# Kernel optimization log

Measured on AMD Instinct MI355X. Metric: run time of the kernel, lower is better.

Reference implementation:

```python
import jax, jax.numpy as jnp
import numpy as np

N = 20000
IN_CH, HID, OUT_CH = 512, 64, 16
H1, H2 = 8, 1
NEG_SLOPE = 0.2


def setup_inputs() -> dict:
    key = jax.random.key(0)
    ks = jax.random.split(key, 10)
    E = 320000
    x = jax.random.normal(ks[0], (N, IN_CH), dtype=jnp.float32)
    edge_index = jax.random.randint(ks[1], (2, E), 0, N, dtype=jnp.int64)
    s = 0.05
    return {
        "x": x,
        "edge_index": edge_index,
        "W1": jax.random.normal(ks[2], (H1 * HID, IN_CH), dtype=jnp.float32) * s,
        "att_src1": jax.random.normal(ks[3], (1, H1, HID), dtype=jnp.float32) * s,
        "att_dst1": jax.random.normal(ks[4], (1, H1, HID), dtype=jnp.float32) * s,
        "b1": jnp.zeros((H1 * HID,), dtype=jnp.float32),
        "W2": jax.random.normal(ks[5], (H2 * OUT_CH, H1 * HID), dtype=jnp.float32) * s,
        "att_src2": jax.random.normal(ks[6], (1, H2, OUT_CH), dtype=jnp.float32) * s,
        "att_dst2": jax.random.normal(ks[7], (1, H2, OUT_CH), dtype=jnp.float32) * s,
        "b2": jnp.zeros((OUT_CH,), dtype=jnp.float32),
    }


def _gat_conv(x, src, dst, W, att_src, att_dst, bias, heads, out_ch, concat):
    # Linear transform: [N, H, C]
    h = (x @ W.T).reshape(x.shape[0], heads, out_ch)
    n = x.shape[0]
    # Per-node attention logits (a_src . h), (a_dst . h): [N, H]
    a_s = (h * att_src).sum(-1)
    a_d = (h * att_dst).sum(-1)
    # Edge-wise LeakyReLU attention: [E, H]
    e = a_s[src] + a_d[dst]
    e = jnp.where(e >= 0, e, NEG_SLOPE * e)
    # Segment softmax over incoming edges of each destination node
    m = jax.ops.segment_max(e, dst, num_segments=n)
    p = jnp.exp(e - m[dst])
    z = jax.ops.segment_sum(p, dst, num_segments=n)
    alpha = p / z[dst]  # [E, H]
    # Weighted scatter-aggregate: out[dst] += alpha * h[src]
    msg = h[src] * alpha[:, :, None]  # [E, H, C]
    out = jax.ops.segment_sum(msg, dst, num_segments=n)
    out = out.reshape(n, heads * out_ch) if concat else out.mean(axis=1)
    return out + bias


def reference(x, edge_index, W1, att_src1, att_dst1, b1, W2, att_src2, att_dst2, b2):
    # PyG GATConv adds self-loops by default
    loops = jnp.arange(N, dtype=edge_index.dtype)
    src = jnp.concatenate([edge_index[0], loops])
    dst = jnp.concatenate([edge_index[1], loops])
    # dropout layers are identity in eval mode
    h = _gat_conv(x, src, dst, W1, att_src1, att_dst1, b1, H1, HID, True)
    h = jax.nn.relu(h)
    out = _gat_conv(h, src, dst, W2, att_src2, att_dst2, b2, H2, OUT_CH, False)
    return out
```

## Files before the change

### kernel.cpp

```cpp
#include <hip/hip_runtime.h>

#define Nn     20000
#define IN_CH  512
#define C1     512
#define H1n    8
#define HIDn   64
#define OUT_CH 16
#define En     320000
#define EPn    340000
#define NEG    0.2f

typedef __attribute__((ext_vector_type(8))) short bf16x8;
typedef __attribute__((ext_vector_type(4))) float f32x4;

__device__ inline unsigned short bf16_rne(float f) {
  unsigned int u = __float_as_uint(f);
  return (unsigned short)((u + 0x7fffu + ((u >> 16) & 1u)) >> 16);
}
__device__ inline float bf16_f(unsigned short u) {
  return __uint_as_float(((unsigned int)u) << 16);
}

#define NX8  (Nn * IN_CH / 8)
#define NW8  (C1 * IN_CH / 8)
#define NW28 (OUT_CH * C1 / 8)
__global__ __launch_bounds__(256) void cvt3_kernel(
    const float* __restrict__ x,  unsigned short* __restrict__ xb,
    const float* __restrict__ W1, unsigned short* __restrict__ w1b,
    const float* __restrict__ W2, unsigned short* __restrict__ w2b)
{
  int i = blockIdx.x * 256 + threadIdx.x;
  const float* in; unsigned short* ob; int idx;
  if (i < NX8) { in = x; ob = xb; idx = i; }
  else if (i < NX8 + NW8) { in = W1; ob = w1b; idx = i - NX8; }
  else if (i < NX8 + NW8 + NW28) { in = W2; ob = w2b; idx = i - NX8 - NW8; }
  else return;
  float4 f0 = ((const float4*)in)[idx * 2];
  float4 f1 = ((const float4*)in)[idx * 2 + 1];
  float f[8] = {f0.x, f0.y, f0.z, f0.w, f1.x, f1.y, f1.z, f1.w};
  unsigned short h[8];
#pragma unroll
  for (int j = 0; j < 8; j++) h[j] = bf16_rne(f[j]);
  ushort4 hv0 = {h[0], h[1], h[2], h[3]}, hv1 = {h[4], h[5], h[6], h[7]};
  ((ushort4*)ob)[idx * 2] = hv0; ((ushort4*)ob)[idx * 2 + 1] = hv1;
}

#define GLL(gp, lp) __builtin_amdgcn_global_load_lds( \
    (const __attribute__((address_space(1))) void*)(gp), \
    (__attribute__((address_space(3))) void*)(lp), 16, 0, 0)

#define SWZ(c) ((c) ^ (((c) >> 3) & 3))

__global__ __launch_bounds__(256, 2) void gemm1_mfma(
    const unsigned short* __restrict__ Ab, const unsigned short* __restrict__ Bb,
    const float* __restrict__ attS, const float* __restrict__ attD,
    unsigned short* __restrict__ Cb, float* __restrict__ as1, float* __restrict__ ad1)
{
  __shared__ unsigned short sA[128 * 32], sB[128 * 32];
  int t = threadIdx.x;
  int bm = blockIdx.x, bn = blockIdx.y;
  int lane = t & 63, w = t >> 6;

  int slot0 = w * 128 + lane;
  int slot1 = slot0 + 64;
  int cb0 = w * 128, cb1 = w * 128 + 64;
  int cs0 = SWZ(slot0), cs1 = SWZ(slot1);
  int ar0 = bm * 128 + (cs0 >> 2); if (ar0 > Nn - 1) ar0 = Nn - 1;
  int ar1 = bm * 128 + (cs1 >> 2); if (ar1 > Nn - 1) ar1 = Nn - 1;
  int br0 = bn * 128 + (cs0 >> 2);
  int br1 = bn * 128 + (cs1 >> 2);
  size_t offA0 = (size_t)ar0 * IN_CH + (cs0 & 3) * 8;
  size_t offA1 = (size_t)ar1 * IN_CH + (cs1 & 3) * 8;
  size_t offB0 = (size_t)br0 * IN_CH + (cs0 & 3) * 8;
  size_t offB1 = (size_t)br1 * IN_CH + (cs1 & 3) * 8;

  int wm = (w >> 1) * 64, wn = (w & 1) * 64;
  int lr = lane & 15, kb = lane >> 4;

  f32x4 acc[4][4] = {};

  for (int k0 = 0; k0 < IN_CH; k0 += 32) {
    __syncthreads();
    GLL(Ab + offA0 + k0, sA + cb0 * 8);
    GLL(Ab + offA1 + k0, sA + cb1 * 8);
    GLL(Bb + offB0 + k0, sB + cb0 * 8);
    GLL(Bb + offB1 + k0, sB + cb1 * 8);
    __syncthreads();

    bf16x8 ah[4], bh[4];
#pragma unroll
    for (int i = 0; i < 4; i++) {
      int rca = (wm + i * 16 + lr) * 4 + kb;
      ah[i] = *(const bf16x8*)&sA[SWZ(rca) * 8];
      int rcb = (wn + i * 16 + lr) * 4 + kb;
      bh[i] = *(const bf16x8*)&sB[SWZ(rcb) * 8];
    }
#pragma unroll
    for (int i = 0; i < 4; i++)
#pragma unroll
      for (int j = 0; j < 4; j++)
        acc[i][j] = __builtin_amdgcn_mfma_f32_16x16x32_bf16(ah[i], bh[j], acc[i][j], 0, 0, 0);
  }

  int lq = lane >> 4;
#pragma unroll
  for (int i = 0; i < 4; i++) {
    int r0 = bm * 128 + wm + i * 16 + lq * 4;
#pragma unroll
    for (int j = 0; j < 4; j++) {
      int cc = bn * 128 + wn + j * 16 + lr;
#pragma unroll
      for (int q = 0; q < 4; q++) {
        int r = r0 + q;
        if (r < Nn) Cb[(size_t)r * C1 + cc] = bf16_rne(acc[i][j][q]);
      }
    }
  }
  int hh = bn * 2 + (wn >> 6);
  float aSj[4], aDj[4];
#pragma unroll
  for (int j = 0; j < 4; j++) {
    int cc = bn * 128 + wn + j * 16 + lr;
    aSj[j] = attS[cc]; aDj[j] = attD[cc];
  }
#pragma unroll
  for (int i = 0; i < 4; i++)
#pragma unroll
    for (int q = 0; q < 4; q++) {
      float s = acc[i][0][q] * aSj[0] + acc[i][1][q] * aSj[1]
              + acc[i][2][q] * aSj[2] + acc[i][3][q] * aSj[3];
      float dd = acc[i][0][q] * aDj[0] + acc[i][1][q] * aDj[1]
               + acc[i][2][q] * aDj[2] + acc[i][3][q] * aDj[3];
#pragma unroll
      for (int off = 1; off < 16; off <<= 1) {
        s += __shfl_xor(s, off);
        dd += __shfl_xor(dd, off);
      }
      int r = bm * 128 + wm + i * 16 + lq * 4 + q;
      if (lr == 0 && r < Nn) { as1[r * 8 + hh] = s; ad1[r * 8 + hh] = dd; }
    }
}

__global__ void hist_kernel(const int* __restrict__ ei, int* __restrict__ cnt)
{
  int e = blockIdx.x * 256 + threadIdx.x;
  if (e >= EPn) return;
  int d = (e < En) ? ei[En + e] : (e - En);
  atomicAdd(&cnt[d], 1);
}

__global__ __launch_bounds__(1024) void scan_kernel(
    const int* __restrict__ cnt, int* __restrict__ row)
{
  __shared__ int wsum[16];
  int t = threadIdx.x;
  int base = t * 20;
  int v[20];
  int s = 0;
#pragma unroll
  for (int j = 0; j < 20; j++) {
    int i = base + j;
    int c = (i < Nn) ? cnt[i] : 0;
    v[j] = s;
    s += c;
  }
  int lane = t & 63, w = t >> 6;
  int incl = s;
#pragma unroll
  for (int off = 1; off < 64; off <<= 1) {
    int o = __shfl_up(incl, off);
    if (lane >= off) incl += o;
  }
  if (lane == 63) wsum[w] = incl;
  __syncthreads();
  if (w == 0) {
    int ws = (lane < 16) ? wsum[lane] : 0;
#pragma unroll
    for (int off = 1; off < 16; off <<= 1) {
      int o = __shfl_up(ws, off);
      if (lane >= off) ws += o;
    }
    if (lane < 16) wsum[lane] = ws;
  }
  __syncthreads();
  int excl = ((w > 0) ? wsum[w - 1] : 0) + incl - s;
#pragma unroll
  for (int j = 0; j < 20; j++) {
    int i = base + j;
    if (i < Nn) row[i] = excl + v[j];
  }
  if (t == 0) row[Nn] = EPn;
}

__global__ void scatter_kernel(const int* __restrict__ ei, const int* __restrict__ row,
                               int* __restrict__ cur, int* __restrict__ csr)
{
  int e = blockIdx.x * 256 + threadIdx.x;
  if (e >= EPn) return;
  int s, d;
  if (e < En) { s = ei[e]; d = ei[En + e]; }
  else        { s = e - En; d = e - En; }
  int pos = row[d] + atomicAdd(&cur[d], 1);
  csr[pos] = s;
}

__global__ __launch_bounds__(256) void agg1_kernel(
    const int* __restrict__ row, const int* __restrict__ csr,
    const unsigned short* __restrict__ h1b, const float* __restrict__ as1,
    const float* __restrict__ adv, const float* __restrict__ b1,
    unsigned short* __restrict__ outb)
{
  int wv = threadIdx.x >> 6, lane = threadIdx.x & 63;
  int d = blockIdx.x * 4 + wv;
  int beg = row[d], end = row[d + 1];
  int hq = lane >> 3;
  size_t chb = (size_t)8 * lane;
  float adH = adv[d * 8 + hq];

  float a0 = 0.f, a1 = 0.f, a2 = 0.f, a3 = 0.f;
  float a4 = 0.f, a5 = 0.f, a6 = 0.f, a7 = 0.f;
  float z = 0.f;
#pragma unroll 4
  for (int e = beg; e < end; e++) {
    int s = csr[e];
    float v = as1[s * 8 + hq] + adH;
    v = (v >= 0.f) ? v : NEG * v;
    float p = __expf(v);
    z += p;
    uint4 u = *(const uint4*)&h1b[(size_t)s * C1 + chb];
    a0 = fmaf(p, __uint_as_float(u.x << 16), a0);
    a1 = fmaf(p, __uint_as_float(u.x & 0xffff0000u), a1);
    a2 = fmaf(p, __uint_as_float(u.y << 16), a2);
    a3 = fmaf(p, __uint_as_float(u.y & 0xffff0000u), a3);
    a4 = fmaf(p, __uint_as_float(u.z << 16), a4);
    a5 = fmaf(p, __uint_as_float(u.z & 0xffff0000u), a5);
    a6 = fmaf(p, __uint_as_float(u.w << 16), a6);
    a7 = fmaf(p, __uint_as_float(u.w & 0xffff0000u), a7);
  }

  float rz = 1.f / z;
  float4 b0 = *(const float4*)&b1[chb];
  float4 b4 = *(const float4*)&b1[chb + 4];
  float o[8] = {fmaf(a0, rz, b0.x), fmaf(a1, rz, b0.y),
                fmaf(a2, rz, b0.z), fmaf(a3, rz, b0.w),
                fmaf(a4, rz, b4.x), fmaf(a5, rz, b4.y),
                fmaf(a6, rz, b4.z), fmaf(a7, rz, b4.w)};
  unsigned short r[8];
#pragma unroll
  for (int i = 0; i < 8; i++) r[i] = bf16_rne(o[i] > 0.f ? o[i] : 0.f);
  ushort4 r0 = {r[0], r[1], r[2], r[3]}, r4 = {r[4], r[5], r[6], r[7]};
  *(ushort4*)&outb[(size_t)d * C1 + chb] = r0;
  *(ushort4*)&outb[(size_t)d * C1 + chb + 4] = r4;
}

__global__ __launch_bounds__(256) void l2_mfma(
    const unsigned short* __restrict__ Xb, const unsigned short* __restrict__ W2b,
    const float* __restrict__ att_s, const float* __restrict__ att_d,
    float* __restrict__ h2, float* __restrict__ as2, float* __restrict__ ad2)
{
  int w = threadIdx.x >> 6, lane = threadIdx.x & 63;
  int tile = blockIdx.x * 4 + w;
  if (tile >= Nn / 16) return;
  int n0 = tile * 16;
  int lr = lane & 15, kb = lane >> 4;

  bf16x8 bf[16];
#pragma unroll
  for (int k0 = 0; k0 < 16; k0++)
    bf[k0] = *(const bf16x8*)&W2b[lr * 512 + kb * 8 + k0 * 32];

  f32x4 acc = {0.f, 0.f, 0.f, 0.f};
#pragma unroll
  for (int k0 = 0; k0 < 16; k0++) {
    bf16x8 af = *(const bf16x8*)&Xb[(size_t)(n0 + lr) * 512 + kb * 8 + k0 * 32];
    acc = __builtin_amdgcn_mfma_f32_16x16x32_bf16(af, bf[k0], acc, 0, 0, 0);
  }

  float aS = att_s[lr], aD = att_d[lr];
#pragma unroll
  for (int r = 0; r < 4; r++) {
    int n = n0 + kb * 4 + r;
    h2[(size_t)n * 16 + lr] = acc[r];
    float sv = acc[r] * aS, dv = acc[r] * aD;
#pragma unroll
    for (int off = 1; off < 16; off <<= 1) {
      sv += __shfl_xor(sv, off);
      dv += __shfl_xor(dv, off);
    }
    if (lr == 0) { as2[n] = sv; ad2[n] = dv; }
  }
}

__global__ __launch_bounds__(256) void agg2_kernel(
    const int* __restrict__ row, const int* __restrict__ csr,
    const float* __restrict__ h2, const float* __restrict__ as2,
    const float* __restrict__ ad2, const float* __restrict__ b2,
    float* __restrict__ out)
{
  int wave = threadIdx.x >> 6, lane = threadIdx.x & 63;
  int d = blockIdx.x * 4 + wave;
  int beg = row[d], end = row[d + 1];
  float add = ad2[d];

  int c = lane & 15;
  float acc = 0.f, z = 0.f;
  for (int e = beg + (lane >> 4); e < end; e += 4) {
    int s = csr[e];
    float v = as2[s] + add;
    v = (v >= 0.f) ? v : NEG * v;
    float p = __expf(v);
    z += p;
    acc = fmaf(p, h2[(size_t)s * 16 + c], acc);
  }
  acc += __shfl_xor(acc, 16);
  acc += __shfl_xor(acc, 32);
  z += __shfl_xor(z, 16);
  z += __shfl_xor(z, 32);
  if (lane < 16) out[(size_t)d * 16 + lane] = acc / z + b2[lane];
}

extern "C" void kernel_launch(void* const* d_in, const int* in_sizes, int n_in,
                              void* d_out, int out_size, void* d_ws, size_t ws_size,
                              hipStream_t stream)
{
  const float* x    = (const float*)d_in[0];
  const int*   ei   = (const int*)d_in[1];
  const float* W1   = (const float*)d_in[2];
  const float* asv1 = (const float*)d_in[3];
  const float* adv1 = (const float*)d_in[4];
  const float* b1   = (const float*)d_in[5];
  const float* W2   = (const float*)d_in[6];
  const float* asv2 = (const float*)d_in[7];
  const float* adv2 = (const float*)d_in[8];
  const float* b2   = (const float*)d_in[9];
  float* out = (float*)d_out;

  unsigned short* h1b    = (unsigned short*)d_ws;
  unsigned short* relu1b = h1b + (size_t)Nn * C1;
  unsigned short* w_b    = relu1b + (size_t)Nn * C1;
  unsigned short* w2b    = w_b + (size_t)C1 * IN_CH;
  float* as1   = (float*)(w2b + (size_t)OUT_CH * C1);
  float* ad1   = as1 + (size_t)Nn * H1n;
  float* h2    = ad1 + (size_t)Nn * H1n;
  float* as2   = h2 + (size_t)Nn * OUT_CH;
  float* ad2   = as2 + Nn;
  int* csr  = (int*)(ad2 + Nn);
  int* cnt  = csr + EPn;
  int* rowp = cnt + Nn;
  int* cur  = rowp + Nn + 1;

  unsigned short* x_b = (unsigned short*)relu1b;

  hipMemsetAsync(cnt, 0, Nn * sizeof(int), stream);
  hipMemsetAsync(cur, 0, Nn * sizeof(int), stream);

  cvt3_kernel<<<(NX8 + NW8 + NW28 + 255) / 256, 256, 0, stream>>>(
      x, x_b, W1, w_b, W2, w2b);

  dim3 g1(157, 4);
  gemm1_mfma<<<g1, 256, 0, stream>>>(x_b, w_b, asv1, adv1, h1b, as1, ad1);

  hist_kernel<<<(EPn + 255) / 256, 256, 0, stream>>>(ei, cnt);
  scan_kernel<<<1, 1024, 0, stream>>>(cnt, rowp);
  scatter_kernel<<<(EPn + 255) / 256, 256, 0, stream>>>(ei, rowp, cur, csr);
  agg1_kernel<<<Nn / 4, 256, 0, stream>>>(rowp, csr, h1b, as1, ad1, b1, relu1b);
  l2_mfma<<<(Nn / 16 + 3) / 4, 256, 0, stream>>>(relu1b, w2b, asv2, adv2, h2, as2, ad2);
  agg2_kernel<<<Nn / 4, 256, 0, stream>>>(rowp, csr, h2, as2, ad2, b2, out);
}
```

Measured before the change: 171.3 us.

## Split each destination's edges across two waves in agg1, merge via LDS

The layer-1 aggregation now gives each destination node two wavefronts that take alternating incoming edges, then combines their partial sums and softmax denominators through shared memory before the wave that owns the node writes the output. The aim is more memory-level parallelism for the latency-bound gather of h1 rows. The cost is twice as many blocks, a block-wide barrier and an LDS round trip. The GEMM1 launch-bounds occupancy hint is also raised from 2 to 3, and the two counter memsets are merged into one by placing the buffers next to each other.

```diff
diff --git a/kernel.cpp b/kernel.cpp
--- a/kernel.cpp
+++ b/kernel.cpp
@@ -51,7 +51,7 @@
 
 #define SWZ(c) ((c) ^ (((c) >> 3) & 3))
 
-__global__ __launch_bounds__(256, 2) void gemm1_mfma(
+__global__ __launch_bounds__(256, 3) void gemm1_mfma(
     const unsigned short* __restrict__ Ab, const unsigned short* __restrict__ Bb,
     const float* __restrict__ attS, const float* __restrict__ attD,
     unsigned short* __restrict__ Cb, float* __restrict__ as1, float* __restrict__ ad1)
@@ -210,9 +210,14 @@
     const float* __restrict__ adv, const float* __restrict__ b1,
     unsigned short* __restrict__ outb)
 {
-  int wv = threadIdx.x >> 6, lane = threadIdx.x & 63;
-  int d = blockIdx.x * 4 + wv;
+  __shared__ float part[2][64 * 9];
+
+  int t = threadIdx.x, lane = t & 63, w = t >> 6;
+  int pr = w >> 1;
+  int p  = w & 1;
+  int d = blockIdx.x * 2 + pr;
   int beg = row[d], end = row[d + 1];
+  int deg = end - beg;
   int hq = lane >> 3;
   size_t chb = (size_t)8 * lane;
   float adH = adv[d * 8 + hq];
@@ -220,37 +225,50 @@
   float a0 = 0.f, a1 = 0.f, a2 = 0.f, a3 = 0.f;
   float a4 = 0.f, a5 = 0.f, a6 = 0.f, a7 = 0.f;
   float z = 0.f;
+  int nj = (deg - p + 1) >> 1;
 #pragma unroll 4
-  for (int e = beg; e < end; e++) {
+  for (int j = 0; j < nj; j++) {
+    int e = beg + p + 2 * j;
     int s = csr[e];
     float v = as1[s * 8 + hq] + adH;
     v = (v >= 0.f) ? v : NEG * v;
-    float p = __expf(v);
-    z += p;
+    float pp = __expf(v);
+    z += pp;
     uint4 u = *(const uint4*)&h1b[(size_t)s * C1 + chb];
-    a0 = fmaf(p, __uint_as_float(u.x << 16), a0);
-    a1 = fmaf(p, __uint_as_float(u.x & 0xffff0000u), a1);
-    a2 = fmaf(p, __uint_as_float(u.y << 16), a2);
-    a3 = fmaf(p, __uint_as_float(u.y & 0xffff0000u), a3);
-    a4 = fmaf(p, __uint_as_float(u.z << 16), a4);
-    a5 = fmaf(p, __uint_as_float(u.z & 0xffff0000u), a5);
-    a6 = fmaf(p, __uint_as_float(u.w << 16), a6);
-    a7 = fmaf(p, __uint_as_float(u.w & 0xffff0000u), a7);
-  }
-
-  float rz = 1.f / z;
-  float4 b0 = *(const float4*)&b1[chb];
-  float4 b4 = *(const float4*)&b1[chb + 4];
-  float o[8] = {fmaf(a0, rz, b0.x), fmaf(a1, rz, b0.y),
-                fmaf(a2, rz, b0.z), fmaf(a3, rz, b0.w),
-                fmaf(a4, rz, b4.x), fmaf(a5, rz, b4.y),
-                fmaf(a6, rz, b4.z), fmaf(a7, rz, b4.w)};
-  unsigned short r[8];
-#pragma unroll
-  for (int i = 0; i < 8; i++) r[i] = bf16_rne(o[i] > 0.f ? o[i] : 0.f);
-  ushort4 r0 = {r[0], r[1], r[2], r[3]}, r4 = {r[4], r[5], r[6], r[7]};
-  *(ushort4*)&outb[(size_t)d * C1 + chb] = r0;
-  *(ushort4*)&outb[(size_t)d * C1 + chb + 4] = r4;
+    a0 = fmaf(pp, __uint_as_float(u.x << 16), a0);
+    a1 = fmaf(pp, __uint_as_float(u.x & 0xffff0000u), a1);
+    a2 = fmaf(pp, __uint_as_float(u.y << 16), a2);
+    a3 = fmaf(pp, __uint_as_float(u.y & 0xffff0000u), a3);
+    a4 = fmaf(pp, __uint_as_float(u.z << 16), a4);
+    a5 = fmaf(pp, __uint_as_float(u.z & 0xffff0000u), a5);
+    a6 = fmaf(pp, __uint_as_float(u.w << 16), a6);
+    a7 = fmaf(pp, __uint_as_float(u.w & 0xffff0000u), a7);
+  }
+
+  if (p == 1) {
+    float* ps = &part[pr][lane * 9];
+    ps[0] = a0; ps[1] = a1; ps[2] = a2; ps[3] = a3;
+    ps[4] = a4; ps[5] = a5; ps[6] = a6; ps[7] = a7; ps[8] = z;
+  }
+  __syncthreads();
+  if (p == 0) {
+    const float* ps = &part[pr][lane * 9];
+    a0 += ps[0]; a1 += ps[1]; a2 += ps[2]; a3 += ps[3];
+    a4 += ps[4]; a5 += ps[5]; a6 += ps[6]; a7 += ps[7]; z += ps[8];
+    float rz = 1.f / z;
+    float4 b0 = *(const float4*)&b1[chb];
+    float4 b4 = *(const float4*)&b1[chb + 4];
+    float o[8] = {fmaf(a0, rz, b0.x), fmaf(a1, rz, b0.y),
+                  fmaf(a2, rz, b0.z), fmaf(a3, rz, b0.w),
+                  fmaf(a4, rz, b4.x), fmaf(a5, rz, b4.y),
+                  fmaf(a6, rz, b4.z), fmaf(a7, rz, b4.w)};
+    unsigned short r[8];
+#pragma unroll
+    for (int i = 0; i < 8; i++) r[i] = bf16_rne(o[i] > 0.f ? o[i] : 0.f);
+    ushort4 r0 = {r[0], r[1], r[2], r[3]}, r4 = {r[4], r[5], r[6], r[7]};
+    *(ushort4*)&outb[(size_t)d * C1 + chb] = r0;
+    *(ushort4*)&outb[(size_t)d * C1 + chb + 4] = r4;
+  }
 }
 
 __global__ __launch_bounds__(256) void l2_mfma(
@@ -346,13 +364,12 @@
   float* ad2   = as2 + Nn;
   int* csr  = (int*)(ad2 + Nn);
   int* cnt  = csr + EPn;
-  int* rowp = cnt + Nn;
-  int* cur  = rowp + Nn + 1;
+  int* cur  = cnt + Nn;
+  int* rowp = cur + Nn;
 
   unsigned short* x_b = (unsigned short*)relu1b;
 
-  hipMemsetAsync(cnt, 0, Nn * sizeof(int), stream);
-  hipMemsetAsync(cur, 0, Nn * sizeof(int), stream);
+  hipMemsetAsync(cnt, 0, 2 * Nn * sizeof(int), stream);
 
   cvt3_kernel<<<(NX8 + NW8 + NW28 + 255) / 256, 256, 0, stream>>>(
       x, x_b, W1, w_b, W2, w2b);
@@ -363,7 +380,7 @@
   hist_kernel<<<(EPn + 255) / 256, 256, 0, stream>>>(ei, cnt);
   scan_kernel<<<1, 1024, 0, stream>>>(cnt, rowp);
   scatter_kernel<<<(EPn + 255) / 256, 256, 0, stream>>>(ei, rowp, cur, csr);
-  agg1_kernel<<<Nn / 4, 256, 0, stream>>>(rowp, csr, h1b, as1, ad1, b1, relu1b);
+  agg1_kernel<<<Nn / 2, 256, 0, stream>>>(rowp, csr, h1b, as1, ad1, b1, relu1b);
   l2_mfma<<<(Nn / 16 + 3) / 4, 256, 0, stream>>>(relu1b, w2b, asv2, adv2, h2, as2, ad2);
   agg2_kernel<<<Nn / 4, 256, 0, stream>>>(rowp, csr, h2, as2, ad2, b2, out);
 }
```

After: 164.5 us. 4.0% less time.
